# Kernel tuning notes

Hardware: AMD Instinct MI355X
Metric: run time of the kernel (lower is better)

## Reference

```python
import jax, jax.numpy as jnp
import numpy as np

SCALE = 0.08838834764831845  # 1/sqrt(128)

def setup_inputs() -> dict:
    key = jax.random.key(0)
    k1, k2, k3 = jax.random.split(key, 3)
    B, H, Lq, Lk, D = 8, 32, 4, 4096, 128
    q = jax.random.normal(k1, (B, H, Lq, D), dtype=jnp.float32)
    k = jax.random.normal(k2, (B, H, Lk, D), dtype=jnp.float32)
    v = jax.random.normal(k3, (B, H, Lk, D), dtype=jnp.float32)
    attention_mask = jnp.zeros((B, 1, Lq, Lk), dtype=jnp.float32)
    return {"q": q, "k": k, "v": v, "attention_mask": attention_mask}

def reference(q, k, v, attention_mask):
    # scores: [B, H, Lq, Lk]
    scores = jnp.einsum('bhqd,bhkd->bhqk', q, k) * SCALE
    scores = scores + attention_mask  # additive mask, broadcasts over H
    weights = jax.nn.softmax(scores, axis=-1)
    out = jnp.einsum('bhqk,bhkd->bhqd', weights, v)  # [B, H, Lq, D]
    return out
```

## Files before the change

kernel.cpp:

```cpp
#include <hip/hip_runtime.h>
#include <math.h>

#define NB   8
#define NH   32
#define LQ   4
#define LK   4096
#define DD   128
#define SCALE_F 0.08838834764831845f

__global__ __launch_bounds__(1024, 4)
void attn_decode_kernel(const float* __restrict__ Q, const float* __restrict__ K,
                        const float* __restrict__ V, const float* __restrict__ Msk,
                        float* __restrict__ Out)
{
    __shared__ float o_buf[16][LQ][DD];
    __shared__ float ml_buf[16][LQ][2];

    const int bh   = blockIdx.x;
    const int b    = bh >> 5;
    const int tid  = threadIdx.x;
    const int wave = tid >> 6;
    const int lane = tid & 63;
    const int half = lane >> 5;
    const int sub  = lane & 31;

    const float* qp = Q   + (size_t)bh * (LQ * DD);
    const float* kp = K   + (size_t)bh * (LK * DD);
    const float* vp = V   + (size_t)bh * (LK * DD);
    const float* mp = Msk + (size_t)b  * (LQ * LK);

    float4 q4[LQ];
#pragma unroll
    for (int qi = 0; qi < LQ; ++qi)
        q4[qi] = *(const float4*)(qp + qi * DD + sub * 4);

    float m_run[LQ], l_run[LQ];
    float4 o4[LQ];
#pragma unroll
    for (int qi = 0; qi < LQ; ++qi) {
        m_run[qi] = -INFINITY;
        l_run[qi] = 0.0f;
        o4[qi].x = 0.0f; o4[qi].y = 0.0f; o4[qi].z = 0.0f; o4[qi].w = 0.0f;
    }

    const int j0 = wave * 256;
    for (int t = 0; t < 256; t += 4) {
        const int ja = j0 + t + half;
        const int jb = ja + 2;

        const float4 ka = *(const float4*)(kp + (size_t)ja * DD + sub * 4);
        const float4 kb = *(const float4*)(kp + (size_t)jb * DD + sub * 4);
        const float4 va = *(const float4*)(vp + (size_t)ja * DD + sub * 4);
        const float4 vb = *(const float4*)(vp + (size_t)jb * DD + sub * 4);

        float sa[LQ], sb[LQ];
#pragma unroll
        for (int qi = 0; qi < LQ; ++qi) {
            sa[qi] = ka.x*q4[qi].x + ka.y*q4[qi].y + ka.z*q4[qi].z + ka.w*q4[qi].w;
            sb[qi] = kb.x*q4[qi].x + kb.y*q4[qi].y + kb.z*q4[qi].z + kb.w*q4[qi].w;
        }
#pragma unroll
        for (int msk = 1; msk <= 16; msk <<= 1) {
#pragma unroll
            for (int qi = 0; qi < LQ; ++qi) {
                sa[qi] += __shfl_xor(sa[qi], msk, 64);
                sb[qi] += __shfl_xor(sb[qi], msk, 64);
            }
        }

#pragma unroll
        for (int qi = 0; qi < LQ; ++qi) {
            const float s_a = sa[qi] * SCALE_F + mp[qi * LK + ja];
            const float s_b = sb[qi] * SCALE_F + mp[qi * LK + jb];
            const float mn  = fmaxf(m_run[qi], fmaxf(s_a, s_b));
            const float f   = __expf(m_run[qi] - mn);
            const float pa  = __expf(s_a - mn);
            const float pb  = __expf(s_b - mn);
            m_run[qi] = mn;
            l_run[qi] = l_run[qi] * f + pa + pb;
            o4[qi].x = o4[qi].x * f + pa * va.x + pb * vb.x;
            o4[qi].y = o4[qi].y * f + pa * va.y + pb * vb.y;
            o4[qi].z = o4[qi].z * f + pa * va.z + pb * vb.z;
            o4[qi].w = o4[qi].w * f + pa * va.w + pb * vb.w;
        }
    }

#pragma unroll
    for (int qi = 0; qi < LQ; ++qi) {
        const float m_o = __shfl_xor(m_run[qi], 32, 64);
        const float l_o = __shfl_xor(l_run[qi], 32, 64);
        float4 oo;
        oo.x = __shfl_xor(o4[qi].x, 32, 64);
        oo.y = __shfl_xor(o4[qi].y, 32, 64);
        oo.z = __shfl_xor(o4[qi].z, 32, 64);
        oo.w = __shfl_xor(o4[qi].w, 32, 64);
        const float M  = fmaxf(m_run[qi], m_o);
        const float fo = __expf(m_run[qi] - M);
        const float fx = __expf(m_o - M);
        o4[qi].x = o4[qi].x * fo + oo.x * fx;
        o4[qi].y = o4[qi].y * fo + oo.y * fx;
        o4[qi].z = o4[qi].z * fo + oo.z * fx;
        o4[qi].w = o4[qi].w * fo + oo.w * fx;
        l_run[qi] = l_run[qi] * fo + l_o * fx;
        m_run[qi] = M;
    }

    if (half == 0) {
#pragma unroll
        for (int qi = 0; qi < LQ; ++qi)
            *(float4*)&o_buf[wave][qi][sub * 4] = o4[qi];
        if (sub == 0) {
#pragma unroll
            for (int qi = 0; qi < LQ; ++qi) {
                ml_buf[wave][qi][0] = m_run[qi];
                ml_buf[wave][qi][1] = l_run[qi];
            }
        }
    }
    __syncthreads();

    if (tid < LQ * DD) {
        const int qi = tid >> 7;
        const int d  = tid & 127;
        float M = -INFINITY;
#pragma unroll
        for (int w = 0; w < 16; ++w)
            M = fmaxf(M, ml_buf[w][qi][0]);
        float Lsum = 0.0f, Osum = 0.0f;
#pragma unroll
        for (int w = 0; w < 16; ++w) {
            const float f = __expf(ml_buf[w][qi][0] - M);
            Lsum += ml_buf[w][qi][1] * f;
            Osum += o_buf[w][qi][d] * f;
        }
        Out[(size_t)bh * (LQ * DD) + tid] = Osum / Lsum;
    }
}

extern "C" void kernel_launch(void* const* d_in, const int* in_sizes, int n_in,
                              void* d_out, int out_size, void* d_ws, size_t ws_size,
                              hipStream_t stream)
{
    const float* q   = (const float*)d_in[0];
    const float* k   = (const float*)d_in[1];
    const float* v   = (const float*)d_in[2];
    const float* msk = (const float*)d_in[3];
    float* out = (float*)d_out;

    attn_decode_kernel<<<dim3(NB * NH), dim3(1024), 0, stream>>>(q, k, v, msk, out);
}
```

Baseline: 206.2 us.

## Split each key row over 16 lanes and prefetch next K/V rows

Each wave now handles four keys at a time: a 16-lane group covers one key row with 8 floats per lane, instead of two 32-lane halves each covering two keys. This cuts the dot-product shuffle reduction from five steps to four and removes one exp per key in the inner loop. K and V for the next iteration are loaded into registers before the current one is consumed, a software prefetch meant to hide global memory latency. The cost is more registers per thread (doubled q and o state plus prefetch buffers) and an extra cross-group merge step at the end.

Result: no change. 206.2 us (-0.0%).

```diff
diff --git a/kernel.cpp b/kernel.cpp
--- a/kernel.cpp
+++ b/kernel.cpp
@@ -21,95 +21,123 @@
     const int tid  = threadIdx.x;
     const int wave = tid >> 6;
     const int lane = tid & 63;
-    const int half = lane >> 5;
-    const int sub  = lane & 31;
+    const int grp  = lane >> 4;
+    const int sl   = lane & 15;
 
     const float* qp = Q   + (size_t)bh * (LQ * DD);
     const float* kp = K   + (size_t)bh * (LK * DD);
     const float* vp = V   + (size_t)bh * (LK * DD);
     const float* mp = Msk + (size_t)b  * (LQ * LK);
 
-    float4 q4[LQ];
+    float4 qa[LQ], qb[LQ];
 #pragma unroll
-    for (int qi = 0; qi < LQ; ++qi)
-        q4[qi] = *(const float4*)(qp + qi * DD + sub * 4);
+    for (int qi = 0; qi < LQ; ++qi) {
+        qa[qi] = *(const float4*)(qp + qi * DD + sl * 8);
+        qb[qi] = *(const float4*)(qp + qi * DD + sl * 8 + 4);
+    }
 
     float m_run[LQ], l_run[LQ];
-    float4 o4[LQ];
+    float4 oa[LQ], ob[LQ];
 #pragma unroll
     for (int qi = 0; qi < LQ; ++qi) {
         m_run[qi] = -INFINITY;
         l_run[qi] = 0.0f;
-        o4[qi].x = 0.0f; o4[qi].y = 0.0f; o4[qi].z = 0.0f; o4[qi].w = 0.0f;
+        oa[qi].x = oa[qi].y = oa[qi].z = oa[qi].w = 0.0f;
+        ob[qi].x = ob[qi].y = ob[qi].z = ob[qi].w = 0.0f;
     }
 
-    const int j0 = wave * 256;
+    const int j0 = wave * 256 + grp;
+
+    const float* kr = kp + (size_t)j0 * DD + sl * 8;
+    const float* vr = vp + (size_t)j0 * DD + sl * 8;
+    float4 ka = *(const float4*)(kr);
+    float4 kb = *(const float4*)(kr + 4);
+    float4 va = *(const float4*)(vr);
+    float4 vb = *(const float4*)(vr + 4);
+
     for (int t = 0; t < 256; t += 4) {
-        const int ja = j0 + t + half;
-        const int jb = ja + 2;
+        const int j = j0 + t;
+        const int jn = j + ((t < 252) ? 4 : 0);
 
-        const float4 ka = *(const float4*)(kp + (size_t)ja * DD + sub * 4);
-        const float4 kb = *(const float4*)(kp + (size_t)jb * DD + sub * 4);
-        const float4 va = *(const float4*)(vp + (size_t)ja * DD + sub * 4);
-        const float4 vb = *(const float4*)(vp + (size_t)jb * DD + sub * 4);
-
-        float sa[LQ], sb[LQ];
+        float s[LQ];
 #pragma unroll
         for (int qi = 0; qi < LQ; ++qi) {
-            sa[qi] = ka.x*q4[qi].x + ka.y*q4[qi].y + ka.z*q4[qi].z + ka.w*q4[qi].w;
-            sb[qi] = kb.x*q4[qi].x + kb.y*q4[qi].y + kb.z*q4[qi].z + kb.w*q4[qi].w;
+            s[qi] = ka.x*qa[qi].x + ka.y*qa[qi].y + ka.z*qa[qi].z + ka.w*qa[qi].w
+                  + kb.x*qb[qi].x + kb.y*qb[qi].y + kb.z*qb[qi].z + kb.w*qb[qi].w;
         }
+
+        const float* krn = kp + (size_t)jn * DD + sl * 8;
+        ka = *(const float4*)(krn);
+        kb = *(const float4*)(krn + 4);
+
 #pragma unroll
-        for (int msk = 1; msk <= 16; msk <<= 1) {
+        for (int msk = 1; msk <= 8; msk <<= 1) {
 #pragma unroll
-            for (int qi = 0; qi < LQ; ++qi) {
-                sa[qi] += __shfl_xor(sa[qi], msk, 64);
-                sb[qi] += __shfl_xor(sb[qi], msk, 64);
-            }
+            for (int qi = 0; qi < LQ; ++qi)
+                s[qi] += __shfl_xor(s[qi], msk, 64);
         }
 
 #pragma unroll
         for (int qi = 0; qi < LQ; ++qi) {
-            const float s_a = sa[qi] * SCALE_F + mp[qi * LK + ja];
-            const float s_b = sb[qi] * SCALE_F + mp[qi * LK + jb];
-            const float mn  = fmaxf(m_run[qi], fmaxf(s_a, s_b));
-            const float f   = __expf(m_run[qi] - mn);
-            const float pa  = __expf(s_a - mn);
-            const float pb  = __expf(s_b - mn);
+            const float sv = s[qi] * SCALE_F + mp[qi * LK + j];
+            const float mn = fmaxf(m_run[qi], sv);
+            const float f  = __expf(m_run[qi] - mn);
+            const float p  = __expf(sv - mn);
             m_run[qi] = mn;
-            l_run[qi] = l_run[qi] * f + pa + pb;
-            o4[qi].x = o4[qi].x * f + pa * va.x + pb * vb.x;
-            o4[qi].y = o4[qi].y * f + pa * va.y + pb * vb.y;
-            o4[qi].z = o4[qi].z * f + pa * va.z + pb * vb.z;
-            o4[qi].w = o4[qi].w * f + pa * va.w + pb * vb.w;
+            l_run[qi] = l_run[qi] * f + p;
+            oa[qi].x = oa[qi].x * f + p * va.x;
+            oa[qi].y = oa[qi].y * f + p * va.y;
+            oa[qi].z = oa[qi].z * f + p * va.z;
+            oa[qi].w = oa[qi].w * f + p * va.w;
+            ob[qi].x = ob[qi].x * f + p * vb.x;
+            ob[qi].y = ob[qi].y * f + p * vb.y;
+            ob[qi].z = ob[qi].z * f + p * vb.z;
+            ob[qi].w = ob[qi].w * f + p * vb.w;
+        }
+
+        const float* vrn = vp + (size_t)jn * DD + sl * 8;
+        va = *(const float4*)(vrn);
+        vb = *(const float4*)(vrn + 4);
+    }
+
+#pragma unroll
+    for (int xm = 16; xm <= 32; xm <<= 1) {
+#pragma unroll
+        for (int qi = 0; qi < LQ; ++qi) {
+            const float m_o = __shfl_xor(m_run[qi], xm, 64);
+            const float l_o = __shfl_xor(l_run[qi], xm, 64);
+            float4 xa, xb;
+            xa.x = __shfl_xor(oa[qi].x, xm, 64);
+            xa.y = __shfl_xor(oa[qi].y, xm, 64);
+            xa.z = __shfl_xor(oa[qi].z, xm, 64);
+            xa.w = __shfl_xor(oa[qi].w, xm, 64);
+            xb.x = __shfl_xor(ob[qi].x, xm, 64);
+            xb.y = __shfl_xor(ob[qi].y, xm, 64);
+            xb.z = __shfl_xor(ob[qi].z, xm, 64);
+            xb.w = __shfl_xor(ob[qi].w, xm, 64);
+            const float M  = fmaxf(m_run[qi], m_o);
+            const float fo = __expf(m_run[qi] - M);
+            const float fx = __expf(m_o - M);
+            oa[qi].x = oa[qi].x * fo + xa.x * fx;
+            oa[qi].y = oa[qi].y * fo + xa.y * fx;
+            oa[qi].z = oa[qi].z * fo + xa.z * fx;
+            oa[qi].w = oa[qi].w * fo + xa.w * fx;
+            ob[qi].x = ob[qi].x * fo + xb.x * fx;
+            ob[qi].y = ob[qi].y * fo + xb.y * fx;
+            ob[qi].z = ob[qi].z * fo + xb.z * fx;
+            ob[qi].w = ob[qi].w * fo + xb.w * fx;
+            l_run[qi] = l_run[qi] * fo + l_o * fx;
+            m_run[qi] = M;
         }
     }
 
+    if (grp == 0) {
 #pragma unroll
-    for (int qi = 0; qi < LQ; ++qi) {
-        const float m_o = __shfl_xor(m_run[qi], 32, 64);
-        const float l_o = __shfl_xor(l_run[qi], 32, 64);
-        float4 oo;
-        oo.x = __shfl_xor(o4[qi].x, 32, 64);
-        oo.y = __shfl_xor(o4[qi].y, 32, 64);
-        oo.z = __shfl_xor(o4[qi].z, 32, 64);
-        oo.w = __shfl_xor(o4[qi].w, 32, 64);
-        const float M  = fmaxf(m_run[qi], m_o);
-        const float fo = __expf(m_run[qi] - M);
-        const float fx = __expf(m_o - M);
-        o4[qi].x = o4[qi].x * fo + oo.x * fx;
-        o4[qi].y = o4[qi].y * fo + oo.y * fx;
-        o4[qi].z = o4[qi].z * fo + oo.z * fx;
-        o4[qi].w = o4[qi].w * fo + oo.w * fx;
-        l_run[qi] = l_run[qi] * fo + l_o * fx;
-        m_run[qi] = M;
-    }
-
-    if (half == 0) {
-#pragma unroll
-        for (int qi = 0; qi < LQ; ++qi)
-            *(float4*)&o_buf[wave][qi][sub * 4] = o4[qi];
-        if (sub == 0) {
+        for (int qi = 0; qi < LQ; ++qi) {
+            *(float4*)&o_buf[wave][qi][sl * 8]     = oa[qi];
+            *(float4*)&o_buf[wave][qi][sl * 8 + 4] = ob[qi];
+        }
+        if (sl == 0) {
 #pragma unroll
             for (int qi = 0; qi < LQ; ++qi) {
                 ml_buf[wave][qi][0] = m_run[qi];
```
